# Kernel tuning notes

Hardware: AMD Instinct MI355X
Metric: run time of the kernel (lower is better)

Reference implementation:

```python
import jax, jax.numpy as jnp
import numpy as np
from jax import lax

# pywt db4 decomposition filters (hardcoded to avoid pywt dependency)
DB4_DEC_LO = np.array([-0.010597401784997278, 0.032883011666982945,
                       0.030841381835986965, -0.18703481171888114,
                       -0.02798376941698385, 0.6308807679295904,
                       0.7148465705525415, 0.23037781330885523], dtype=np.float32)
DB4_DEC_HI = np.array([-0.23037781330885523, 0.7148465705525415,
                       -0.6308807679295904, -0.02798376941698385,
                       0.18703481171888114, 0.030841381835986965,
                       -0.032883011666982945, -0.010597401784997278], dtype=np.float32)

B, T, C = 32, 16384, 64

def setup_inputs() -> dict:
    key = jax.random.key(0)
    x = jax.random.normal(key, (B, T, C), dtype=jnp.float32)
    return {"x": x,
            "dec_lo": jnp.asarray(DB4_DEC_LO),
            "dec_hi": jnp.asarray(DB4_DEC_HI)}

def _depthwise_conv1d(xp, filt, channels):
    # xp: [B, L, C]; filt: [K]; depthwise stride-2 valid cross-correlation
    k = jnp.broadcast_to(filt[:, None, None], (filt.shape[0], 1, channels))  # [K,1,C]
    return lax.conv_general_dilated(
        xp, k, window_strides=(2,), padding='VALID',
        dimension_numbers=('NWC', 'WIO', 'NWC'),
        feature_group_count=channels)

def reference(x, dec_lo, dec_hi):
    channels = x.shape[-1]
    filter_length = dec_lo.shape[0]          # 8 for db4
    pad = filter_length - 1                   # 7
    crop = pad // 2                           # 3
    xp = jnp.pad(x, ((0, 0), (pad, pad), (0, 0)), mode='reflect')
    approx = _depthwise_conv1d(xp, dec_lo, channels)[:, crop:-crop, :]
    detail = _depthwise_conv1d(xp, dec_hi, channels)[:, crop:-crop, :]
    # original concatenates all approx channels then all detail channels
    return jnp.concatenate([approx, detail], axis=-1)  # [B, T/2-2, 2C]
```

## Files before the change

kernel.cpp:

```cpp
#include <hip/hip_runtime.h>


#define BT    32
#define TT    16384
#define CC    64
#define T2    8190
#define OC    128
#define NQUAD 2048

__global__ __launch_bounds__(256, 4) void dwt_db4_quad_kernel(
    const float* __restrict__ x,
    const float* __restrict__ dec_lo,
    const float* __restrict__ dec_hi,
    float* __restrict__ out)
{
    const int tid  = threadIdx.x;
    const int cg   = tid & 15;
    const int tq   = tid >> 4;
    const int quad = blockIdx.x * 16 + tq;
    const int b    = blockIdx.y;

    const int t0 = quad * 4;
    const int c4 = cg * 4;
    const int m0 = 2 * t0 - 1;

    const float* __restrict__ xb = x + (size_t)b * TT * CC;

    float4 w[14];
    if (m0 >= 0 && m0 + 13 <= TT - 1) {
        const float* __restrict__ p = xb + (size_t)m0 * CC + c4;
        #pragma unroll
        for (int i = 0; i < 14; ++i)
            w[i] = *reinterpret_cast<const float4*>(p + i * CC);
    } else {
        #pragma unroll
        for (int i = 0; i < 14; ++i) {
            int m  = m0 + i;
            int mm = m < 0 ? -m : m;
            mm     = mm > (TT - 1) ? 2 * (TT - 1) - mm : mm;
            w[i] = *reinterpret_cast<const float4*>(xb + (size_t)mm * CC + c4);
        }
    }

    float flo[8], fhi[8];
    #pragma unroll
    for (int k = 0; k < 8; ++k) { flo[k] = dec_lo[k]; fhi[k] = dec_hi[k]; }

    float4 alo[4], ahi[4];
    #pragma unroll
    for (int i = 0; i < 4; ++i) {
        alo[i].x = alo[i].y = alo[i].z = alo[i].w = 0.0f;
        ahi[i].x = ahi[i].y = ahi[i].z = ahi[i].w = 0.0f;
    }

    #pragma unroll
    for (int k = 0; k < 8; ++k) {
        #pragma unroll
        for (int i = 0; i < 4; ++i) {
            const float4 v = w[2 * i + k];
            alo[i].x = fmaf(flo[k], v.x, alo[i].x);
            alo[i].y = fmaf(flo[k], v.y, alo[i].y);
            alo[i].z = fmaf(flo[k], v.z, alo[i].z);
            alo[i].w = fmaf(flo[k], v.w, alo[i].w);
            ahi[i].x = fmaf(fhi[k], v.x, ahi[i].x);
            ahi[i].y = fmaf(fhi[k], v.y, ahi[i].y);
            ahi[i].z = fmaf(fhi[k], v.z, ahi[i].z);
            ahi[i].w = fmaf(fhi[k], v.w, ahi[i].w);
        }
    }

    float* __restrict__ ob = out + (size_t)b * T2 * OC + (size_t)t0 * OC + c4;
    if (t0 + 4 <= T2) {
        #pragma unroll
        for (int i = 0; i < 4; ++i) {
            *reinterpret_cast<float4*>(ob + i * OC)      = alo[i];
            *reinterpret_cast<float4*>(ob + i * OC + CC) = ahi[i];
        }
    } else {
        #pragma unroll
        for (int i = 0; i < 4; ++i) {
            if (t0 + i < T2) {
                *reinterpret_cast<float4*>(ob + i * OC)      = alo[i];
                *reinterpret_cast<float4*>(ob + i * OC + CC) = ahi[i];
            }
        }
    }
}

extern "C" void kernel_launch(void* const* d_in, const int* in_sizes, int n_in,
                              void* d_out, int out_size, void* d_ws, size_t ws_size,
                              hipStream_t stream)
{
    const float* x      = (const float*)d_in[0];
    const float* dec_lo = (const float*)d_in[1];
    const float* dec_hi = (const float*)d_in[2];
    float*       out    = (float*)d_out;

    dim3 block(256);
    dim3 grid(NQUAD / 16, BT);

    hipLaunchKernelGGL(dwt_db4_quad_kernel, grid, block, 0, stream,
                       x, dec_lo, dec_hi, out);
}
```

Measured before the change: 243.9 us.

## Stage input rows in LDS via global_load_lds and read windows from shared memory

Each block now cooperatively copies the 136 input rows it needs into LDS with direct global-to-LDS loads, then each thread reads its 14-row window from LDS instead of global memory. This removes the redundant overlapping global reads between neighbouring time quads, which the old kernel left to the cache. In exchange it adds 34 KB of shared memory per block, a barrier, and reflect-index arithmetic on every LDS read. Occupancy may drop as a result.

```diff
diff --git a/kernel.cpp b/kernel.cpp
--- a/kernel.cpp
+++ b/kernel.cpp
@@ -1,50 +1,66 @@
 #include <hip/hip_runtime.h>
 
 
-#define BT    32
-#define TT    16384
-#define CC    64
-#define T2    8190
-#define OC    128
-#define NQUAD 2048
+#define BT     32
+#define TT     16384
+#define CC     64
+#define T2     8190
+#define OC     128
+#define TBLK   64
+#define NROWS  136
+#define NCHUNK 34
 
-__global__ __launch_bounds__(256, 4) void dwt_db4_quad_kernel(
+__global__ __launch_bounds__(256, 4) void dwt_db4_lds_kernel(
     const float* __restrict__ x,
     const float* __restrict__ dec_lo,
     const float* __restrict__ dec_hi,
     float* __restrict__ out)
 {
-    const int tid  = threadIdx.x;
-    const int cg   = tid & 15;
-    const int tq   = tid >> 4;
-    const int quad = blockIdx.x * 16 + tq;
-    const int b    = blockIdx.y;
+    __shared__ float lds[NROWS * CC];
 
-    const int t0 = quad * 4;
-    const int c4 = cg * 4;
-    const int m0 = 2 * t0 - 1;
+    const int tid = threadIdx.x;
+    const int b   = blockIdx.y;
+    const int t0  = blockIdx.x * TBLK;
+    const int row_base = (t0 == 0) ? 0 : (2 * t0 - 1);
 
     const float* __restrict__ xb = x + (size_t)b * TT * CC;
 
-    float4 w[14];
-    if (m0 >= 0 && m0 + 13 <= TT - 1) {
-        const float* __restrict__ p = xb + (size_t)m0 * CC + c4;
+    {
+        const int wave = tid >> 6;
+        const int lane = tid & 63;
+        const float* gsrc = xb + (size_t)row_base * CC + lane * 4;
+        const float* gend = xb + (size_t)TT * CC - 4;
         #pragma unroll
-        for (int i = 0; i < 14; ++i)
-            w[i] = *reinterpret_cast<const float4*>(p + i * CC);
-    } else {
-        #pragma unroll
-        for (int i = 0; i < 14; ++i) {
-            int m  = m0 + i;
-            int mm = m < 0 ? -m : m;
-            mm     = mm > (TT - 1) ? 2 * (TT - 1) - mm : mm;
-            w[i] = *reinterpret_cast<const float4*>(xb + (size_t)mm * CC + c4);
+        for (int c = wave; c < NCHUNK; c += 4) {
+            const float* g = gsrc + c * 256;
+            g = (g > gend) ? gend : g;
+            __builtin_amdgcn_global_load_lds(
+                (const __attribute__((address_space(1))) unsigned int*)g,
+                (__attribute__((address_space(3))) unsigned int*)&lds[c * 256],
+                16, 0, 0);
         }
     }
 
     float flo[8], fhi[8];
     #pragma unroll
     for (int k = 0; k < 8; ++k) { flo[k] = dec_lo[k]; fhi[k] = dec_hi[k]; }
+
+    __syncthreads();
+
+    const int cg = tid & 15;
+    const int tq = tid >> 4;
+    const int t  = t0 + tq * 4;
+    const int c4 = cg * 4;
+
+    float4 w[14];
+    #pragma unroll
+    for (int i = 0; i < 14; ++i) {
+        int m  = 2 * t - 1 + i;
+        int mm = m < 0 ? -m : m;
+        mm     = mm > (TT - 1) ? 2 * (TT - 1) - mm : mm;
+        int lr = mm - row_base;
+        w[i] = *reinterpret_cast<const float4*>(&lds[lr * CC + c4]);
+    }
 
     float4 alo[4], ahi[4];
     #pragma unroll
@@ -69,20 +85,12 @@
         }
     }
 
-    float* __restrict__ ob = out + (size_t)b * T2 * OC + (size_t)t0 * OC + c4;
-    if (t0 + 4 <= T2) {
-        #pragma unroll
-        for (int i = 0; i < 4; ++i) {
+    float* __restrict__ ob = out + (size_t)b * T2 * OC + (size_t)t * OC + c4;
+    #pragma unroll
+    for (int i = 0; i < 4; ++i) {
+        if (t + i < T2) {
             *reinterpret_cast<float4*>(ob + i * OC)      = alo[i];
             *reinterpret_cast<float4*>(ob + i * OC + CC) = ahi[i];
-        }
-    } else {
-        #pragma unroll
-        for (int i = 0; i < 4; ++i) {
-            if (t0 + i < T2) {
-                *reinterpret_cast<float4*>(ob + i * OC)      = alo[i];
-                *reinterpret_cast<float4*>(ob + i * OC + CC) = ahi[i];
-            }
         }
     }
 }
@@ -97,8 +105,8 @@
     float*       out    = (float*)d_out;
 
     dim3 block(256);
-    dim3 grid(NQUAD / 16, BT);
+    dim3 grid((T2 + TBLK - 1) / TBLK, BT);
 
-    hipLaunchKernelGGL(dwt_db4_quad_kernel, grid, block, 0, stream,
+    hipLaunchKernelGGL(dwt_db4_lds_kernel, grid, block, 0, stream,
                        x, dec_lo, dec_hi, out);
 }
```

New measurement: 234.8 us. 1.04x faster.

## Restructure DWT kernel into a grid-stride loop with software-pipelined asm loads

Applied to the files above, without the earlier changes.

Replaces the one-quad-per-thread kernel with a fixed 1024-block grid. Each thread handles eight output-pair items and double-buffers their input windows. The loads are issued as inline-asm global_load_dwordx4 with manual s_waitcnt, so the next item's loads are in flight while the current one is computed and stored. Filter taps are forced to scalar registers via readfirstlane. The cost is more redundant input reads per output (10 rows per 2 outputs instead of 14 per 4), and correctness depends on the hand-written vmcnt counts staying valid while stores share the same counter.

```diff
diff --git a/kernel.cpp b/kernel.cpp
--- a/kernel.cpp
+++ b/kernel.cpp
@@ -1,89 +1,124 @@
 #include <hip/hip_runtime.h>
+#include <stdint.h>
 
 
-#define BT    32
-#define TT    16384
-#define CC    64
-#define T2    8190
-#define OC    128
-#define NQUAD 2048
+typedef float f32x4 __attribute__((ext_vector_type(4)));
 
-__global__ __launch_bounds__(256, 4) void dwt_db4_quad_kernel(
+#define BT       32
+#define TT       16384
+#define CC       64
+#define T2       8190
+#define OC       128
+#define PAIR_SL  4096
+#define NT       262144
+#define KIT      8
+
+struct Item {
+    const float* src;
+    float*       dst;
+    int          t;
+    bool         valid;
+};
+
+__device__ __forceinline__ Item decode(int g, const float* __restrict__ x,
+                                       float* __restrict__ out)
+{
+    const int cg   = g & 15;
+    const int pair = (g >> 4) & (PAIR_SL - 1);
+    const int b    = g >> 16;
+    Item it;
+    it.t     = pair * 2;
+    it.src   = x   + (size_t)b * TT * CC + cg * 4;
+    it.dst   = out + (size_t)b * T2 * OC + (size_t)(pair * 2) * OC + cg * 4;
+    it.valid = pair < (PAIR_SL - 1);
+    return it;
+}
+
+__device__ __forceinline__ void issue10(const Item& it, f32x4 (&w)[10])
+{
+    #pragma unroll
+    for (int i = 0; i < 10; ++i) {
+        int m  = 2 * it.t - 1 + i;
+        int mm = m < 0 ? -m : m;
+        mm     = mm > (TT - 1) ? 2 * (TT - 1) - mm : mm;
+        const uint64_t a = (uint64_t)(it.src + (size_t)mm * CC);
+        asm volatile("global_load_dwordx4 %0, %1, off"
+                     : "=v"(w[i]) : "v"(a) : "memory");
+    }
+}
+
+__device__ __forceinline__ void compute_store(const f32x4 (&w)[10],
+                                              const Item& it,
+                                              const float* __restrict__ flo,
+                                              const float* __restrict__ fhi)
+{
+    if (!it.valid) return;
+    f32x4* ob = (f32x4*)it.dst;
+    f32x4 a;
+
+    a = flo[0] * w[0];
+    #pragma unroll
+    for (int k = 1; k < 8; ++k) a += flo[k] * w[k];
+    ob[0] = a;
+
+    a = fhi[0] * w[0];
+    #pragma unroll
+    for (int k = 1; k < 8; ++k) a += fhi[k] * w[k];
+    ob[16] = a;
+
+    a = flo[0] * w[2];
+    #pragma unroll
+    for (int k = 1; k < 8; ++k) a += flo[k] * w[k + 2];
+    ob[32] = a;
+
+    a = fhi[0] * w[2];
+    #pragma unroll
+    for (int k = 1; k < 8; ++k) a += fhi[k] * w[k + 2];
+    ob[48] = a;
+}
+
+__global__ __launch_bounds__(256, 4) void dwt_db4_stream_kernel(
     const float* __restrict__ x,
     const float* __restrict__ dec_lo,
     const float* __restrict__ dec_hi,
     float* __restrict__ out)
 {
-    const int tid  = threadIdx.x;
-    const int cg   = tid & 15;
-    const int tq   = tid >> 4;
-    const int quad = blockIdx.x * 16 + tq;
-    const int b    = blockIdx.y;
-
-    const int t0 = quad * 4;
-    const int c4 = cg * 4;
-    const int m0 = 2 * t0 - 1;
-
-    const float* __restrict__ xb = x + (size_t)b * TT * CC;
-
-    float4 w[14];
-    if (m0 >= 0 && m0 + 13 <= TT - 1) {
-        const float* __restrict__ p = xb + (size_t)m0 * CC + c4;
-        #pragma unroll
-        for (int i = 0; i < 14; ++i)
-            w[i] = *reinterpret_cast<const float4*>(p + i * CC);
-    } else {
-        #pragma unroll
-        for (int i = 0; i < 14; ++i) {
-            int m  = m0 + i;
-            int mm = m < 0 ? -m : m;
-            mm     = mm > (TT - 1) ? 2 * (TT - 1) - mm : mm;
-            w[i] = *reinterpret_cast<const float4*>(xb + (size_t)mm * CC + c4);
-        }
-    }
+    const int tid = blockIdx.x * 256 + threadIdx.x;
 
     float flo[8], fhi[8];
     #pragma unroll
-    for (int k = 0; k < 8; ++k) { flo[k] = dec_lo[k]; fhi[k] = dec_hi[k]; }
-
-    float4 alo[4], ahi[4];
-    #pragma unroll
-    for (int i = 0; i < 4; ++i) {
-        alo[i].x = alo[i].y = alo[i].z = alo[i].w = 0.0f;
-        ahi[i].x = ahi[i].y = ahi[i].z = ahi[i].w = 0.0f;
+    for (int k = 0; k < 8; ++k) {
+        flo[k] = __int_as_float(
+            __builtin_amdgcn_readfirstlane(__float_as_int(dec_lo[k])));
+        fhi[k] = __int_as_float(
+            __builtin_amdgcn_readfirstlane(__float_as_int(dec_hi[k])));
     }
 
+    f32x4 wA[10], wB[10];
+
+    int gA = tid;
+    Item iA = decode(gA, x, out);
+    issue10(iA, wA);
+
     #pragma unroll
-    for (int k = 0; k < 8; ++k) {
-        #pragma unroll
-        for (int i = 0; i < 4; ++i) {
-            const float4 v = w[2 * i + k];
-            alo[i].x = fmaf(flo[k], v.x, alo[i].x);
-            alo[i].y = fmaf(flo[k], v.y, alo[i].y);
-            alo[i].z = fmaf(flo[k], v.z, alo[i].z);
-            alo[i].w = fmaf(flo[k], v.w, alo[i].w);
-            ahi[i].x = fmaf(fhi[k], v.x, ahi[i].x);
-            ahi[i].y = fmaf(fhi[k], v.y, ahi[i].y);
-            ahi[i].z = fmaf(fhi[k], v.z, ahi[i].z);
-            ahi[i].w = fmaf(fhi[k], v.w, ahi[i].w);
+    for (int k = 0; k < KIT / 2; ++k) {
+        const int gB = gA + NT;
+        Item iB = decode(gB, x, out);
+        issue10(iB, wB);
+        asm volatile("s_waitcnt vmcnt(10)" ::: "memory");
+        __builtin_amdgcn_sched_barrier(0);
+        compute_store(wA, iA, flo, fhi);
+
+        if (k < KIT / 2 - 1) {
+            gA = gB + NT;
+            iA = decode(gA, x, out);
+            issue10(iA, wA);
+            asm volatile("s_waitcnt vmcnt(10)" ::: "memory");
+        } else {
+            asm volatile("s_waitcnt vmcnt(0)" ::: "memory");
         }
-    }
-
-    float* __restrict__ ob = out + (size_t)b * T2 * OC + (size_t)t0 * OC + c4;
-    if (t0 + 4 <= T2) {
-        #pragma unroll
-        for (int i = 0; i < 4; ++i) {
-            *reinterpret_cast<float4*>(ob + i * OC)      = alo[i];
-            *reinterpret_cast<float4*>(ob + i * OC + CC) = ahi[i];
-        }
-    } else {
-        #pragma unroll
-        for (int i = 0; i < 4; ++i) {
-            if (t0 + i < T2) {
-                *reinterpret_cast<float4*>(ob + i * OC)      = alo[i];
-                *reinterpret_cast<float4*>(ob + i * OC + CC) = ahi[i];
-            }
-        }
+        __builtin_amdgcn_sched_barrier(0);
+        compute_store(wB, iB, flo, fhi);
     }
 }
 
@@ -97,8 +132,8 @@
     float*       out    = (float*)d_out;
 
     dim3 block(256);
-    dim3 grid(NQUAD / 16, BT);
+    dim3 grid(NT / 256);
 
-    hipLaunchKernelGGL(dwt_db4_quad_kernel, grid, block, 0, stream,
+    hipLaunchKernelGGL(dwt_db4_stream_kernel, grid, block, 0, stream,
                        x, dec_lo, dec_hi, out);
 }
```

New measurement: 231.8 us. -4.9%, faster.
